# Kernel tuning notes

Hardware: AMD Instinct MI355X
Metric: run time of the kernel (lower is better)

The kernel has to match this reference:

```python
import jax, jax.numpy as jnp
import numpy as np
import math

B, S, HID = 128, 200, 1024
NH = 4
DK = HID // NH
LSESS = 200  # session_len
MAXSEQ = 200
EPS = 1e-12


def setup_inputs() -> dict:
    key = jax.random.key(0)
    ks = jax.random.split(key, 12)
    inp = {}
    inp['query'] = jax.random.normal(ks[0], (B, S, HID), jnp.float32)
    inp['key'] = jax.random.normal(ks[1], (B, S, HID), jnp.float32)
    inp['value'] = jax.random.normal(ks[2], (B, S, HID), jnp.float32)
    std = 0.05
    inp['attn_w0'] = std * jax.random.normal(ks[3], (DK, DK), jnp.float32)
    inp['attn_w1'] = std * jax.random.normal(ks[4], (DK, DK), jnp.float32)
    inp['attn_w2'] = std * jax.random.normal(ks[5], (DK, DK), jnp.float32)
    inp['attn_w3'] = std * jax.random.normal(ks[6], (LSESS, DK), jnp.float32)
    inp['attn_bias'] = jnp.zeros((DK,), jnp.float32)
    inp['complex_weight'] = 0.02 * jax.random.normal(ks[7], (1, NH, MAXSEQ // 2 + 1, DK, 2), jnp.float32)
    bound = 1.0 / math.sqrt(HID)
    inp['linear_w'] = jax.random.uniform(ks[8], (HID, HID), jnp.float32, -bound, bound)
    inp['linear_b'] = jax.random.uniform(ks[9], (HID,), jnp.float32, -bound, bound)
    inp['ln_w'] = jnp.ones((HID,), jnp.float32)
    inp['ln_b'] = jnp.zeros((HID,), jnp.float32)
    return inp


def _gelu(x):
    return x * 0.5 * (1.0 + jax.lax.erf(x / jnp.sqrt(jnp.asarray(2.0, x.dtype))))


def reference(query, key, value, attn_w0, attn_w1, attn_w2, attn_w3, attn_bias,
              complex_weight, linear_w, linear_b, ln_w, ln_b):
    nb = query.shape[0]
    # (B, S, H, DK) -> (B, H, S, DK)
    def split_heads(x):
        return x.reshape(nb, -1, NH, DK).transpose(0, 2, 1, 3)
    q, k, v = split_heads(query), split_heads(key), split_heads(value)

    q = q @ attn_w0
    k = k @ attn_w1
    v = v @ attn_w2

    qf = jnp.fft.rfft(q, axis=2, norm='ortho')   # (B,H,S//2+1,DK) complex
    kf = jnp.fft.rfft(k, axis=2, norm='ortho')
    weight = complex_weight[..., 0] + 1j * complex_weight[..., 1]  # (1,4,MAXSEQ//2+1,DK)
    res = qf * jnp.conj(kf) * weight
    corr = jnp.fft.irfft(res, n=MAXSEQ, axis=2, norm='ortho')       # (B,H,MAXSEQ,DK)

    alpha = jnp.matmul(jax.nn.relu(corr + attn_bias), attn_w3.T)    # (B,H,MAXSEQ,LSESS)
    alpha = jax.nn.softmax(alpha, axis=-2)                          # softmax over seq dim
    x = jnp.einsum('bhsl,bhsd->bhld', alpha, v)                     # (B,H,LSESS,DK)

    x = x.transpose(0, 2, 1, 3).reshape(nb, -1, NH * DK)            # (B,LSESS,HID)
    x = x @ linear_w.T + linear_b
    # dropout is identity at inference
    x = _gelu(x)
    # LayerNorm (TF-style, eps inside sqrt)
    u = x.mean(-1, keepdims=True)
    s = ((x - u) ** 2).mean(-1, keepdims=True)
    x = (x - u) / jnp.sqrt(s + EPS)
    return ln_w * x + ln_b
```

## Files before the change

### kernel.cpp

```cpp
#include <hip/hip_runtime.h>
#include <hip/hip_bf16.h>
#include <math.h>

#define BATCH 128
#define SEQ   200
#define HID   1024
#define NH    4
#define DK    256
#define NF    101
#define NF2   202
#define LS    200
#define PD    256

typedef __attribute__((ext_vector_type(8))) short bf16x8;
typedef __attribute__((ext_vector_type(4))) float f32x4;

__device__ __forceinline__ unsigned short f2bf(float f) {
    union { float f; unsigned u; } v; v.f = f;
    unsigned r = v.u + 0x7fff + ((v.u >> 16) & 1);
    return (unsigned short)(r >> 16);
}
__device__ __forceinline__ float bf2f(unsigned short h) {
    union { unsigned u; float f; } v; v.u = ((unsigned)h) << 16;
    return v.f;
}

__device__ __forceinline__ void gld_lds16(const void* g, void* l) {
    __builtin_amdgcn_global_load_lds(
        (const __attribute__((address_space(1))) unsigned*)g,
        (__attribute__((address_space(3))) unsigned*)l, 16, 0, 0);
}

__global__ void init_tables_bf16(unsigned short* __restrict__ F, unsigned short* __restrict__ G) {
    int idx = blockIdx.x * 256 + threadIdx.x;
    const double inv = 0.07071067811865475244;
    const double PI2 = 6.283185307179586476925;
    {
        int fidx = idx >> 8, s = idx & 255;
        double v = 0.0;
        if (s < SEQ && fidx < NF2) {
            int f = (fidx < NF) ? fidx : fidx - NF;
            double ang = PI2 * (double)((f * s) % SEQ) / (double)SEQ;
            v = (fidx < NF) ? cos(ang) * inv : -sin(ang) * inv;
        }
        F[idx] = f2bf((float)v);
    }
    {
        int s = idx >> 8, j = idx & 255;
        double v = 0.0;
        if (s < SEQ && j < NF2) {
            if (j < NF) {
                double al = (j == 0 || j == NF - 1) ? 1.0 : 2.0;
                v = al * cos(PI2 * (double)((j * s) % SEQ) / (double)SEQ) * inv;
            } else {
                int f = j - NF;
                if (f != 0 && f != NF - 1)
                    v = -2.0 * sin(PI2 * (double)((f * s) % SEQ) / (double)SEQ) * inv;
            }
        }
        G[idx] = f2bf((float)v);
    }
}

__global__ void wtrans256(const float* __restrict__ src, unsigned short* __restrict__ dst) {
    int dout = blockIdx.x, din = threadIdx.x;
    dst[dout * 256 + din] = f2bf(src[din * 256 + dout]);
}

__global__ void w3pad(const float* __restrict__ src, unsigned short* __restrict__ dst) {
    int row = blockIdx.x, col = threadIdx.x;
    dst[row * 256 + col] = (row < LS) ? f2bf(src[row * 256 + col]) : (unsigned short)0;
}

__global__ void fconv(const float* __restrict__ src, unsigned short* __restrict__ dst, int n) {
    int i = blockIdx.x * 256 + threadIdx.x;
    if (i < n) dst[i] = f2bf(src[i]);
}

template <bool B_F32, int EPI>
__global__ __launch_bounds__(256)
void mgemm128(const void* __restrict__ Av, const void* __restrict__ Bv, void* __restrict__ Cv,
              int K, int lda, int ldb, int ldc,
              long aOuter, long aInner, long bOuter, long bInner,
              long cOuter, long cInner, int nInner, int nbValid,
              const float* __restrict__ biasN) {
    int bz = blockIdx.z;
    int bo = bz / nInner, bi = bz - bo * nInner;
    const unsigned short* A = (const unsigned short*)Av + bo * aOuter + bi * aInner;
    const unsigned short* Bh = nullptr;
    const float* Bf = nullptr;
    if (B_F32) Bf = (const float*)Bv + bo * bOuter + bi * bInner;
    else       Bh = (const unsigned short*)Bv + bo * bOuter + bi * bInner;

    __shared__ unsigned short As[128 * 64];
    __shared__ unsigned short Bs[128 * 64];

    int t = threadIdx.x;
    int m0 = blockIdx.y * 128, n0 = blockIdx.x * 128;
    int lane = t & 63, wave = t >> 6;
    int wr = wave >> 1, wc = wave & 1;
    int la = lane & 15, hi = lane >> 4;

    f32x4 acc[4][4] = {};

    int rsub = t >> 3;
    int c8 = (t & 7) * 8;

    for (int k0 = 0; k0 < K; k0 += 64) {
#pragma unroll
        for (int p = 0; p < 4; ++p) {
            int row = p * 32 + rsub;
            gld_lds16(A + (long)(m0 + row) * lda + k0 + c8, &As[row * 64 + c8]);
        }
        if (!B_F32) {
#pragma unroll
            for (int p = 0; p < 4; ++p) {
                int row = p * 32 + rsub;
                gld_lds16(Bh + (long)(n0 + row) * ldb + k0 + c8, &Bs[row * 64 + c8]);
            }
        } else {
#pragma unroll
            for (int p = 0; p < 4; ++p) {
                int row = p * 32 + rsub;
                int gn = n0 + row;
                unsigned short tmp[8];
                if (gn < nbValid) {
                    const float4* src = reinterpret_cast<const float4*>(Bf + (long)gn * ldb + k0 + c8);
                    float4 x0 = src[0], x1 = src[1];
                    tmp[0] = f2bf(x0.x); tmp[1] = f2bf(x0.y); tmp[2] = f2bf(x0.z); tmp[3] = f2bf(x0.w);
                    tmp[4] = f2bf(x1.x); tmp[5] = f2bf(x1.y); tmp[6] = f2bf(x1.z); tmp[7] = f2bf(x1.w);
                } else {
#pragma unroll
                    for (int j = 0; j < 8; ++j) tmp[j] = 0;
                }
                *(bf16x8*)&Bs[row * 64 + c8] = *(bf16x8*)tmp;
            }
        }
        __syncthreads();
#pragma unroll
        for (int half = 0; half < 2; ++half) {
            int ko = half * 32 + hi * 8;
            bf16x8 a[4], b[4];
#pragma unroll
            for (int mi = 0; mi < 4; ++mi)
                a[mi] = *(const bf16x8*)&As[(wr * 64 + mi * 16 + la) * 64 + ko];
#pragma unroll
            for (int ni = 0; ni < 4; ++ni)
                b[ni] = *(const bf16x8*)&Bs[(wc * 64 + ni * 16 + la) * 64 + ko];
#pragma unroll
            for (int mi = 0; mi < 4; ++mi)
#pragma unroll
                for (int ni = 0; ni < 4; ++ni)
                    acc[mi][ni] = __builtin_amdgcn_mfma_f32_16x16x32_bf16(a[mi], b[ni], acc[mi][ni], 0, 0, 0);
        }
        __syncthreads();
    }

    unsigned short* Ch = nullptr; float* Cf = nullptr;
    if (EPI == 1 || EPI == 3) Cf = (float*)Cv + bo * cOuter + bi * cInner;
    else                      Ch = (unsigned short*)Cv + bo * cOuter + bi * cInner;

#pragma unroll
    for (int mi = 0; mi < 4; ++mi) {
#pragma unroll
        for (int ni = 0; ni < 4; ++ni) {
            int gn = n0 + wc * 64 + ni * 16 + la;
            int gmB = m0 + wr * 64 + mi * 16 + hi * 4;
            float bN = 0.f;
            if (EPI == 2 || EPI == 3) bN = biasN[gn];
#pragma unroll
            for (int rr = 0; rr < 4; ++rr) {
                float v = acc[mi][ni][rr];
                long idx = (long)(gmB + rr) * ldc + gn;
                if (EPI == 0) Ch[idx] = f2bf(v);
                else if (EPI == 1) Cf[idx] = v;
                else if (EPI == 2) Ch[idx] = f2bf(fmaxf(v + bN, 0.f));
                else Cf[idx] = v + bN;
            }
        }
    }
}

__global__ void crossspec(unsigned short* __restrict__ QF, const unsigned short* __restrict__ KF,
                          const float* __restrict__ cw) {
    long idx = (long)blockIdx.x * 256 + threadIdx.x;
    if (idx >= (long)BATCH * NH * DK * NF) return;
    int f = (int)(idx % NF);
    long tq = idx / NF;
    int d = (int)(tq % DK);
    int bh = (int)(tq / DK);
    int h = bh & (NH - 1);
    long base = (long)bh * DK * PD + (long)d * PD;
    float qr = bf2f(QF[base + f]), qi = bf2f(QF[base + NF + f]);
    float kr = bf2f(KF[base + f]), ki = bf2f(KF[base + NF + f]);
    float cr = qr * kr + qi * ki;
    float ci = qi * kr - qr * ki;
    long wb = (((long)h * NF + f) * DK + d) * 2;
    float wr = cw[wb], wi = cw[wb + 1];
    QF[base + f]      = f2bf(cr * wr - ci * wi);
    QF[base + NF + f] = f2bf(cr * wi + ci * wr);
    if (f < PD - NF2) QF[base + NF2 + f] = 0;
}

__global__ __launch_bounds__(256) void softmax_rows(const float* __restrict__ in,
                                                    unsigned short* __restrict__ out) {
    long row = (long)blockIdx.x * 4 + (threadIdx.x >> 6);
    int lane = threadIdx.x & 63;
    const float* p = in + row * PD;
    float v[4];
    float m = -1e30f;
#pragma unroll
    for (int i = 0; i < 4; ++i) {
        int s = lane + 64 * i;
        v[i] = (s < SEQ) ? p[s] : -1e30f;
        m = fmaxf(m, v[i]);
    }
#pragma unroll
    for (int o = 32; o; o >>= 1) m = fmaxf(m, __shfl_xor(m, o));
    float e[4], sum = 0.f;
#pragma unroll
    for (int i = 0; i < 4; ++i) {
        int s = lane + 64 * i;
        e[i] = (s < SEQ) ? expf(v[i] - m) : 0.f;
        sum += e[i];
    }
#pragma unroll
    for (int o = 32; o; o >>= 1) sum += __shfl_xor(sum, o);
    float inv = 1.f / sum;
    unsigned short* q = out + row * PD;
#pragma unroll
    for (int i = 0; i < 4; ++i) {
        int s = lane + 64 * i;
        q[s] = (s < SEQ) ? f2bf(e[i] * inv) : (unsigned short)0;
    }
}

__global__ __launch_bounds__(256) void transposeX(const unsigned short* __restrict__ xT,
                                                  unsigned short* __restrict__ X) {
    __shared__ unsigned short T[64][72];
    int bh = blockIdx.z, d0 = blockIdx.y * 64, l0 = blockIdx.x * 64;
    int b = bh >> 2, h = bh & 3;
    int t = threadIdx.x;
    int r = t >> 2, seg = (t & 3) * 16;
    const unsigned short* src = xT + (long)bh * PD * PD + (long)(d0 + r) * PD + l0 + seg;
    *(bf16x8*)&T[r][seg]     = *(const bf16x8*)(src);
    *(bf16x8*)&T[r][seg + 8] = *(const bf16x8*)(src + 8);
    __syncthreads();
    int l = l0 + r;
    if (l < LS) {
        unsigned short* dst = X + ((long)b * LS + l) * HID + h * DK + d0 + seg;
#pragma unroll
        for (int j = 0; j < 16; ++j) dst[j] = T[seg + j][r];
    }
}

__global__ __launch_bounds__(256) void gelu_ln_kernel(const float* __restrict__ y2,
                               const float* __restrict__ lnw, const float* __restrict__ lnb,
                               float* __restrict__ out) {
    long row = blockIdx.x;
    const float4* xr = reinterpret_cast<const float4*>(y2 + row * HID);
    int tid = threadIdx.x;
    float4 v4 = xr[tid];
    float g[4];
    g[0] = 0.5f * v4.x * (1.f + erff(v4.x * 0.70710678118654752f));
    g[1] = 0.5f * v4.y * (1.f + erff(v4.y * 0.70710678118654752f));
    g[2] = 0.5f * v4.z * (1.f + erff(v4.z * 0.70710678118654752f));
    g[3] = 0.5f * v4.w * (1.f + erff(v4.w * 0.70710678118654752f));

    __shared__ float red[4];
    float s = g[0] + g[1] + g[2] + g[3];
#pragma unroll
    for (int o = 32; o > 0; o >>= 1) s += __shfl_down(s, o);
    if ((tid & 63) == 0) red[tid >> 6] = s;
    __syncthreads();
    float mean = (red[0] + red[1] + red[2] + red[3]) * (1.f / (float)HID);

    float v2 = 0.f;
#pragma unroll
    for (int p = 0; p < 4; ++p) { float d = g[p] - mean; v2 += d * d; }
    __syncthreads();
#pragma unroll
    for (int o = 32; o > 0; o >>= 1) v2 += __shfl_down(v2, o);
    if ((tid & 63) == 0) red[tid >> 6] = v2;
    __syncthreads();
    float var = (red[0] + red[1] + red[2] + red[3]) * (1.f / (float)HID);
    float rstd = rsqrtf(var + 1e-12f);

    float4 o4;
    int i0 = tid * 4;
    o4.x = (g[0] - mean) * rstd * lnw[i0 + 0] + lnb[i0 + 0];
    o4.y = (g[1] - mean) * rstd * lnw[i0 + 1] + lnb[i0 + 1];
    o4.z = (g[2] - mean) * rstd * lnw[i0 + 2] + lnb[i0 + 2];
    o4.w = (g[3] - mean) * rstd * lnw[i0 + 3] + lnb[i0 + 3];
    reinterpret_cast<float4*>(out + row * HID)[tid] = o4;
}

extern "C" void kernel_launch(void* const* d_in, const int* in_sizes, int n_in,
                              void* d_out, int out_size, void* d_ws, size_t ws_size,
                              hipStream_t stream) {
    const float* query = (const float*)d_in[0];
    const float* key   = (const float*)d_in[1];
    const float* value = (const float*)d_in[2];
    const float* w0 = (const float*)d_in[3];
    const float* w1 = (const float*)d_in[4];
    const float* w2 = (const float*)d_in[5];
    const float* w3 = (const float*)d_in[6];
    const float* attn_bias = (const float*)d_in[7];
    const float* cw = (const float*)d_in[8];
    const float* lw = (const float*)d_in[9];
    const float* lb = (const float*)d_in[10];
    const float* lnw = (const float*)d_in[11];
    const float* lnb = (const float*)d_in[12];
    float* out = (float*)d_out;

    char* base = (char*)d_ws;
    const long BH = (long)BATCH * NH;
    const long SZR = (long)BH * PD * PD;
    const size_t M64 = 67108864;

    unsigned short* F_stack = (unsigned short*)(base + 0);
    unsigned short* G_stack = (unsigned short*)(base + 131072);
    unsigned short* w0T = (unsigned short*)(base + 262144);
    unsigned short* w1T = (unsigned short*)(base + 393216);
    unsigned short* w2T = (unsigned short*)(base + 524288);
    unsigned short* w3b = (unsigned short*)(base + 655360);
    unsigned short* lwb = (unsigned short*)(base + 786432);
    char* rA = base + 4194304;
    char* rB = rA + M64;
    char* rC = rB + M64;
    char* rD = rC + M64;
    char* rE = rD + M64;

    unsigned short* qpT = (unsigned short*)rA;
    unsigned short* kpT = (unsigned short*)rB;
    unsigned short* vpT = (unsigned short*)rC;
    unsigned short* QF  = (unsigned short*)rD;
    unsigned short* KF  = (unsigned short*)rE;
    unsigned short* corr = (unsigned short*)rA;
    float*          alphaT = (float*)rD;
    unsigned short* probs = (unsigned short*)rB;
    unsigned short* xT = (unsigned short*)rE;
    unsigned short* X  = (unsigned short*)rA;
    float*          y2 = (float*)rD;

    init_tables_bf16<<<256, 256, 0, stream>>>(F_stack, G_stack);
    wtrans256<<<256, 256, 0, stream>>>(w0, w0T);
    wtrans256<<<256, 256, 0, stream>>>(w1, w1T);
    wtrans256<<<256, 256, 0, stream>>>(w2, w2T);
    w3pad<<<256, 256, 0, stream>>>(w3, w3b);
    fconv<<<(HID * HID + 255) / 256, 256, 0, stream>>>(lw, lwb, HID * HID);

    dim3 gproj(2, 2, BH);
    mgemm128<true, 0><<<gproj, 256, 0, stream>>>(w0T, query, qpT, DK, DK, HID, PD,
        0L, 0L, (long)SEQ * HID, (long)DK, (long)NH * PD * PD, (long)PD * PD, NH, SEQ, nullptr);
    mgemm128<true, 0><<<gproj, 256, 0, stream>>>(w1T, key, kpT, DK, DK, HID, PD,
        0L, 0L, (long)SEQ * HID, (long)DK, (long)NH * PD * PD, (long)PD * PD, NH, SEQ, nullptr);
    mgemm128<true, 0><<<gproj, 256, 0, stream>>>(w2T, value, vpT, DK, DK, HID, PD,
        0L, 0L, (long)SEQ * HID, (long)DK, (long)NH * PD * PD, (long)PD * PD, NH, SEQ, nullptr);

    dim3 gfwd(2, 2, 2 * BH);
    mgemm128<false, 0><<<gfwd, 256, 0, stream>>>(qpT, F_stack, QF, PD, PD, PD, PD,
        SZR, (long)PD * PD, 0L, 0L, SZR, (long)PD * PD, (int)BH, PD, nullptr);

    long ncs = (long)BH * DK * NF;
    crossspec<<<(unsigned)((ncs + 255) / 256), 256, 0, stream>>>(QF, KF, cw);

    dim3 gstd(2, 2, BH);
    mgemm128<false, 2><<<gstd, 256, 0, stream>>>(G_stack, QF, corr, PD, PD, PD, PD,
        0L, 0L, (long)PD * PD, 0L, (long)PD * PD, 0L, 1, PD, attn_bias);

    mgemm128<false, 1><<<gstd, 256, 0, stream>>>(w3b, corr, alphaT, PD, PD, PD, PD,
        0L, 0L, (long)PD * PD, 0L, (long)PD * PD, 0L, 1, PD, nullptr);

    softmax_rows<<<(unsigned)(BH * PD / 4), 256, 0, stream>>>(alphaT, probs);

    mgemm128<false, 0><<<gstd, 256, 0, stream>>>(vpT, probs, xT, PD, PD, PD, PD,
        (long)PD * PD, 0L, (long)PD * PD, 0L, (long)PD * PD, 0L, 1, PD, nullptr);

    transposeX<<<dim3(4, 4, BH), 256, 0, stream>>>(xT, X);

    dim3 glin(HID / 128, (BATCH * LS) / 128, 1);
    mgemm128<false, 3><<<glin, 256, 0, stream>>>(X, lwb, y2, HID, HID, HID, HID,
        0L, 0L, 0L, 0L, 0L, 0L, 1, HID, lb);

    gelu_ln_kernel<<<(unsigned)(BATCH * LS), 256, 0, stream>>>(y2, lnw, lnb, out);
}
```

Before: 720.5 us.

## Double-buffer bf16 GEMMs, fuse transpose into attention GEMM, store intermediates as bf16

Adds a double-buffered LDS GEMM variant that prefetches the next K tile while computing the current one. It switches alpha and the linear output from fp32 to bf16 storage, which halves their memory traffic. The value GEMM is reordered to write directly in (B,LS,HID) layout, so the separate transpose kernel is no longer needed. The big linear GEMM gets an XCD-aware block swizzle. The costs are lower precision on the softmax input and on the GELU/LN input, plus twice the shared memory per block.

```diff
diff --git a/kernel.cpp b/kernel.cpp
--- a/kernel.cpp
+++ b/kernel.cpp
@@ -77,20 +77,16 @@
     if (i < n) dst[i] = f2bf(src[i]);
 }
 
-template <bool B_F32, int EPI>
 __global__ __launch_bounds__(256)
-void mgemm128(const void* __restrict__ Av, const void* __restrict__ Bv, void* __restrict__ Cv,
+void mgemm128(const unsigned short* __restrict__ A, const float* __restrict__ Bf0,
+              unsigned short* __restrict__ C0,
               int K, int lda, int ldb, int ldc,
               long aOuter, long aInner, long bOuter, long bInner,
-              long cOuter, long cInner, int nInner, int nbValid,
-              const float* __restrict__ biasN) {
+              long cOuter, long cInner, int nInner, int nbValid) {
     int bz = blockIdx.z;
     int bo = bz / nInner, bi = bz - bo * nInner;
-    const unsigned short* A = (const unsigned short*)Av + bo * aOuter + bi * aInner;
-    const unsigned short* Bh = nullptr;
-    const float* Bf = nullptr;
-    if (B_F32) Bf = (const float*)Bv + bo * bOuter + bi * bInner;
-    else       Bh = (const unsigned short*)Bv + bo * bOuter + bi * bInner;
+    const unsigned short* Ab = A + bo * aOuter + bi * aInner;
+    const float* Bf = Bf0 + bo * bOuter + bi * bInner;
 
     __shared__ unsigned short As[128 * 64];
     __shared__ unsigned short Bs[128 * 64];
@@ -102,7 +98,6 @@
     int la = lane & 15, hi = lane >> 4;
 
     f32x4 acc[4][4] = {};
-
     int rsub = t >> 3;
     int c8 = (t & 7) * 8;
 
@@ -110,31 +105,23 @@
 #pragma unroll
         for (int p = 0; p < 4; ++p) {
             int row = p * 32 + rsub;
-            gld_lds16(A + (long)(m0 + row) * lda + k0 + c8, &As[row * 64 + c8]);
-        }
-        if (!B_F32) {
-#pragma unroll
-            for (int p = 0; p < 4; ++p) {
-                int row = p * 32 + rsub;
-                gld_lds16(Bh + (long)(n0 + row) * ldb + k0 + c8, &Bs[row * 64 + c8]);
+            gld_lds16(Ab + (long)(m0 + row) * lda + k0 + c8, &As[row * 64 + c8]);
+        }
+#pragma unroll
+        for (int p = 0; p < 4; ++p) {
+            int row = p * 32 + rsub;
+            int gn = n0 + row;
+            unsigned short tmp[8];
+            if (gn < nbValid) {
+                const float4* src = reinterpret_cast<const float4*>(Bf + (long)gn * ldb + k0 + c8);
+                float4 x0 = src[0], x1 = src[1];
+                tmp[0] = f2bf(x0.x); tmp[1] = f2bf(x0.y); tmp[2] = f2bf(x0.z); tmp[3] = f2bf(x0.w);
+                tmp[4] = f2bf(x1.x); tmp[5] = f2bf(x1.y); tmp[6] = f2bf(x1.z); tmp[7] = f2bf(x1.w);
+            } else {
+#pragma unroll
+                for (int j = 0; j < 8; ++j) tmp[j] = 0;
             }
-        } else {
-#pragma unroll
-            for (int p = 0; p < 4; ++p) {
-                int row = p * 32 + rsub;
-                int gn = n0 + row;
-                unsigned short tmp[8];
-                if (gn < nbValid) {
-                    const float4* src = reinterpret_cast<const float4*>(Bf + (long)gn * ldb + k0 + c8);
-                    float4 x0 = src[0], x1 = src[1];
-                    tmp[0] = f2bf(x0.x); tmp[1] = f2bf(x0.y); tmp[2] = f2bf(x0.z); tmp[3] = f2bf(x0.w);
-                    tmp[4] = f2bf(x1.x); tmp[5] = f2bf(x1.y); tmp[6] = f2bf(x1.z); tmp[7] = f2bf(x1.w);
-                } else {
-#pragma unroll
-                    for (int j = 0; j < 8; ++j) tmp[j] = 0;
-                }
-                *(bf16x8*)&Bs[row * 64 + c8] = *(bf16x8*)tmp;
-            }
+            *(bf16x8*)&Bs[row * 64 + c8] = *(bf16x8*)tmp;
         }
         __syncthreads();
 #pragma unroll
@@ -156,10 +143,96 @@
         __syncthreads();
     }
 
-    unsigned short* Ch = nullptr; float* Cf = nullptr;
-    if (EPI == 1 || EPI == 3) Cf = (float*)Cv + bo * cOuter + bi * cInner;
-    else                      Ch = (unsigned short*)Cv + bo * cOuter + bi * cInner;
-
+    unsigned short* Ch = C0 + bo * cOuter + bi * cInner;
+#pragma unroll
+    for (int mi = 0; mi < 4; ++mi) {
+#pragma unroll
+        for (int ni = 0; ni < 4; ++ni) {
+            int gn = n0 + wc * 64 + ni * 16 + la;
+            int gmB = m0 + wr * 64 + mi * 16 + hi * 4;
+#pragma unroll
+            for (int rr = 0; rr < 4; ++rr)
+                Ch[(long)(gmB + rr) * ldc + gn] = f2bf(acc[mi][ni][rr]);
+        }
+    }
+}
+
+template <int EPI, bool XCDSWZ>
+__global__ __launch_bounds__(256)
+void mgemm128p(const unsigned short* __restrict__ A, const unsigned short* __restrict__ B,
+               unsigned short* __restrict__ C0, int K, int lda, int ldb, int ldc,
+               long aOuter, long aInner, long bOuter, long bInner,
+               long cOuter, long cInner, int nInner, int mValid,
+               const float* __restrict__ biasN) {
+    int bx = blockIdx.x, by = blockIdx.y;
+    if (XCDSWZ) {
+        int nwg = gridDim.x * gridDim.y;
+        int flat = by * gridDim.x + bx;
+        int cpx = nwg >> 3;
+        int swz = (flat & 7) * cpx + (flat >> 3);
+        bx = swz % gridDim.x; by = swz / gridDim.x;
+    }
+    int bz = blockIdx.z;
+    int bo = bz / nInner, bi = bz - bo * nInner;
+    const unsigned short* Ab = A + bo * aOuter + bi * aInner;
+    const unsigned short* Bb = B + bo * bOuter + bi * bInner;
+
+    __shared__ unsigned short As[2][128 * 64];
+    __shared__ unsigned short Bs[2][128 * 64];
+
+    int t = threadIdx.x;
+    int m0 = by * 128, n0 = bx * 128;
+    int lane = t & 63, wave = t >> 6;
+    int wr = wave >> 1, wc = wave & 1;
+    int la = lane & 15, hi = lane >> 4;
+
+    f32x4 acc[4][4] = {};
+    int rsub = t >> 3;
+    int c8 = (t & 7) * 8;
+
+    int ktiles = K >> 6;
+
+#pragma unroll
+    for (int p = 0; p < 4; ++p) {
+        int row = p * 32 + rsub;
+        gld_lds16(Ab + (long)(m0 + row) * lda + c8, &As[0][row * 64 + c8]);
+        gld_lds16(Bb + (long)(n0 + row) * ldb + c8, &Bs[0][row * 64 + c8]);
+    }
+    __syncthreads();
+
+    int cur = 0;
+    for (int kt = 0; kt < ktiles; ++kt) {
+        if (kt + 1 < ktiles) {
+            int k0 = (kt + 1) << 6;
+            int nxt = cur ^ 1;
+#pragma unroll
+            for (int p = 0; p < 4; ++p) {
+                int row = p * 32 + rsub;
+                gld_lds16(Ab + (long)(m0 + row) * lda + k0 + c8, &As[nxt][row * 64 + c8]);
+                gld_lds16(Bb + (long)(n0 + row) * ldb + k0 + c8, &Bs[nxt][row * 64 + c8]);
+            }
+        }
+#pragma unroll
+        for (int half = 0; half < 2; ++half) {
+            int ko = half * 32 + hi * 8;
+            bf16x8 a[4], b[4];
+#pragma unroll
+            for (int mi = 0; mi < 4; ++mi)
+                a[mi] = *(const bf16x8*)&As[cur][(wr * 64 + mi * 16 + la) * 64 + ko];
+#pragma unroll
+            for (int ni = 0; ni < 4; ++ni)
+                b[ni] = *(const bf16x8*)&Bs[cur][(wc * 64 + ni * 16 + la) * 64 + ko];
+#pragma unroll
+            for (int mi = 0; mi < 4; ++mi)
+#pragma unroll
+                for (int ni = 0; ni < 4; ++ni)
+                    acc[mi][ni] = __builtin_amdgcn_mfma_f32_16x16x32_bf16(a[mi], b[ni], acc[mi][ni], 0, 0, 0);
+        }
+        __syncthreads();
+        cur ^= 1;
+    }
+
+    unsigned short* Ch = C0 + bo * cOuter + bi * cInner;
 #pragma unroll
     for (int mi = 0; mi < 4; ++mi) {
 #pragma unroll
@@ -167,15 +240,15 @@
             int gn = n0 + wc * 64 + ni * 16 + la;
             int gmB = m0 + wr * 64 + mi * 16 + hi * 4;
             float bN = 0.f;
-            if (EPI == 2 || EPI == 3) bN = biasN[gn];
+            if (EPI == 2 || EPI == 4) bN = biasN[gn];
 #pragma unroll
             for (int rr = 0; rr < 4; ++rr) {
+                int gm = gmB + rr;
+                if (gm >= mValid) continue;
                 float v = acc[mi][ni][rr];
-                long idx = (long)(gmB + rr) * ldc + gn;
-                if (EPI == 0) Ch[idx] = f2bf(v);
-                else if (EPI == 1) Cf[idx] = v;
-                else if (EPI == 2) Ch[idx] = f2bf(fmaxf(v + bN, 0.f));
-                else Cf[idx] = v + bN;
+                if (EPI == 0) Ch[(long)gm * ldc + gn] = f2bf(v);
+                else if (EPI == 2) Ch[(long)gm * ldc + gn] = f2bf(fmaxf(v + bN, 0.f));
+                else Ch[(long)gm * ldc + gn] = f2bf(v + bN);
             }
         }
     }
@@ -202,17 +275,17 @@
     if (f < PD - NF2) QF[base + NF2 + f] = 0;
 }
 
-__global__ __launch_bounds__(256) void softmax_rows(const float* __restrict__ in,
+__global__ __launch_bounds__(256) void softmax_rows(const unsigned short* __restrict__ in,
                                                     unsigned short* __restrict__ out) {
     long row = (long)blockIdx.x * 4 + (threadIdx.x >> 6);
     int lane = threadIdx.x & 63;
-    const float* p = in + row * PD;
+    const unsigned short* p = in + row * PD;
     float v[4];
     float m = -1e30f;
 #pragma unroll
     for (int i = 0; i < 4; ++i) {
         int s = lane + 64 * i;
-        v[i] = (s < SEQ) ? p[s] : -1e30f;
+        v[i] = (s < SEQ) ? bf2f(p[s]) : -1e30f;
         m = fmaxf(m, v[i]);
     }
 #pragma unroll
@@ -235,37 +308,22 @@
     }
 }
 
-__global__ __launch_bounds__(256) void transposeX(const unsigned short* __restrict__ xT,
-                                                  unsigned short* __restrict__ X) {
-    __shared__ unsigned short T[64][72];
-    int bh = blockIdx.z, d0 = blockIdx.y * 64, l0 = blockIdx.x * 64;
-    int b = bh >> 2, h = bh & 3;
-    int t = threadIdx.x;
-    int r = t >> 2, seg = (t & 3) * 16;
-    const unsigned short* src = xT + (long)bh * PD * PD + (long)(d0 + r) * PD + l0 + seg;
-    *(bf16x8*)&T[r][seg]     = *(const bf16x8*)(src);
-    *(bf16x8*)&T[r][seg + 8] = *(const bf16x8*)(src + 8);
-    __syncthreads();
-    int l = l0 + r;
-    if (l < LS) {
-        unsigned short* dst = X + ((long)b * LS + l) * HID + h * DK + d0 + seg;
-#pragma unroll
-        for (int j = 0; j < 16; ++j) dst[j] = T[seg + j][r];
-    }
-}
-
-__global__ __launch_bounds__(256) void gelu_ln_kernel(const float* __restrict__ y2,
+__global__ __launch_bounds__(256) void gelu_ln_kernel(const unsigned short* __restrict__ y2,
                                const float* __restrict__ lnw, const float* __restrict__ lnb,
                                float* __restrict__ out) {
     long row = blockIdx.x;
-    const float4* xr = reinterpret_cast<const float4*>(y2 + row * HID);
     int tid = threadIdx.x;
-    float4 v4 = xr[tid];
+    const short4* xr = reinterpret_cast<const short4*>(y2 + row * HID);
+    short4 h4 = xr[tid];
     float g[4];
-    g[0] = 0.5f * v4.x * (1.f + erff(v4.x * 0.70710678118654752f));
-    g[1] = 0.5f * v4.y * (1.f + erff(v4.y * 0.70710678118654752f));
-    g[2] = 0.5f * v4.z * (1.f + erff(v4.z * 0.70710678118654752f));
-    g[3] = 0.5f * v4.w * (1.f + erff(v4.w * 0.70710678118654752f));
+    {
+        float x0 = bf2f((unsigned short)h4.x), x1 = bf2f((unsigned short)h4.y);
+        float x2 = bf2f((unsigned short)h4.z), x3 = bf2f((unsigned short)h4.w);
+        g[0] = 0.5f * x0 * (1.f + erff(x0 * 0.70710678118654752f));
+        g[1] = 0.5f * x1 * (1.f + erff(x1 * 0.70710678118654752f));
+        g[2] = 0.5f * x2 * (1.f + erff(x2 * 0.70710678118654752f));
+        g[3] = 0.5f * x3 * (1.f + erff(x3 * 0.70710678118654752f));
+    }
 
     __shared__ float red[4];
     float s = g[0] + g[1] + g[2] + g[3];
@@ -337,11 +395,10 @@
     unsigned short* QF  = (unsigned short*)rD;
     unsigned short* KF  = (unsigned short*)rE;
     unsigned short* corr = (unsigned short*)rA;
-    float*          alphaT = (float*)rD;
+    unsigned short* alphaT = (unsigned short*)rD;
     unsigned short* probs = (unsigned short*)rB;
-    unsigned short* xT = (unsigned short*)rE;
-    unsigned short* X  = (unsigned short*)rA;
-    float*          y2 = (float*)rD;
+    unsigned short* X  = (unsigned short*)rE;
+    unsigned short* y2 = (unsigned short*)rD;
 
     init_tables_bf16<<<256, 256, 0, stream>>>(F_stack, G_stack);
     wtrans256<<<256, 256, 0, stream>>>(w0, w0T);
@@ -351,37 +408,37 @@
     fconv<<<(HID * HID + 255) / 256, 256, 0, stream>>>(lw, lwb, HID * HID);
 
     dim3 gproj(2, 2, BH);
-    mgemm128<true, 0><<<gproj, 256, 0, stream>>>(w0T, query, qpT, DK, DK, HID, PD,
-        0L, 0L, (long)SEQ * HID, (long)DK, (long)NH * PD * PD, (long)PD * PD, NH, SEQ, nullptr);
-    mgemm128<true, 0><<<gproj, 256, 0, stream>>>(w1T, key, kpT, DK, DK, HID, PD,
-        0L, 0L, (long)SEQ * HID, (long)DK, (long)NH * PD * PD, (long)PD * PD, NH, SEQ, nullptr);
-    mgemm128<true, 0><<<gproj, 256, 0, stream>>>(w2T, value, vpT, DK, DK, HID, PD,
-        0L, 0L, (long)SEQ * HID, (long)DK, (long)NH * PD * PD, (long)PD * PD, NH, SEQ, nullptr);
+    mgemm128<<<gproj, 256, 0, stream>>>(w0T, query, qpT, DK, DK, HID, PD,
+        0L, 0L, (long)SEQ * HID, (long)DK, (long)NH * PD * PD, (long)PD * PD, NH, SEQ);
+    mgemm128<<<gproj, 256, 0, stream>>>(w1T, key, kpT, DK, DK, HID, PD,
+        0L, 0L, (long)SEQ * HID, (long)DK, (long)NH * PD * PD, (long)PD * PD, NH, SEQ);
+    mgemm128<<<gproj, 256, 0, stream>>>(w2T, value, vpT, DK, DK, HID, PD,
+        0L, 0L, (long)SEQ * HID, (long)DK, (long)NH * PD * PD, (long)PD * PD, NH, SEQ);
 
     dim3 gfwd(2, 2, 2 * BH);
-    mgemm128<false, 0><<<gfwd, 256, 0, stream>>>(qpT, F_stack, QF, PD, PD, PD, PD,
+    mgemm128p<0, false><<<gfwd, 256, 0, stream>>>(qpT, F_stack, QF, PD, PD, PD, PD,
         SZR, (long)PD * PD, 0L, 0L, SZR, (long)PD * PD, (int)BH, PD, nullptr);
 
     long ncs = (long)BH * DK * NF;
     crossspec<<<(unsigned)((ncs + 255) / 256), 256, 0, stream>>>(QF, KF, cw);
 
     dim3 gstd(2, 2, BH);
-    mgemm128<false, 2><<<gstd, 256, 0, stream>>>(G_stack, QF, corr, PD, PD, PD, PD,
+    mgemm128p<2, false><<<gstd, 256, 0, stream>>>(G_stack, QF, corr, PD, PD, PD, PD,
         0L, 0L, (long)PD * PD, 0L, (long)PD * PD, 0L, 1, PD, attn_bias);
 
-    mgemm128<false, 1><<<gstd, 256, 0, stream>>>(w3b, corr, alphaT, PD, PD, PD, PD,
+    mgemm128p<0, false><<<gstd, 256, 0, stream>>>(w3b, corr, alphaT, PD, PD, PD, PD,
         0L, 0L, (long)PD * PD, 0L, (long)PD * PD, 0L, 1, PD, nullptr);
 
     softmax_rows<<<(unsigned)(BH * PD / 4), 256, 0, stream>>>(alphaT, probs);
 
-    mgemm128<false, 0><<<gstd, 256, 0, stream>>>(vpT, probs, xT, PD, PD, PD, PD,
-        (long)PD * PD, 0L, (long)PD * PD, 0L, (long)PD * PD, 0L, 1, PD, nullptr);
-
-    transposeX<<<dim3(4, 4, BH), 256, 0, stream>>>(xT, X);
+    mgemm128p<0, false><<<gstd, 256, 0, stream>>>(probs, vpT, X, PD, PD, PD, HID,
+        (long)NH * PD * PD, (long)PD * PD,
+        (long)NH * PD * PD, (long)PD * PD,
+        (long)LS * HID, (long)DK, NH, LS, nullptr);
 
     dim3 glin(HID / 128, (BATCH * LS) / 128, 1);
-    mgemm128<false, 3><<<glin, 256, 0, stream>>>(X, lwb, y2, HID, HID, HID, HID,
-        0L, 0L, 0L, 0L, 0L, 0L, 1, HID, lb);
+    mgemm128p<4, true><<<glin, 256, 0, stream>>>(X, lwb, y2, HID, HID, HID, HID,
+        0L, 0L, 0L, 0L, 0L, 0L, 1, BATCH * LS, lb);
 
     gelu_ln_kernel<<<(unsigned)(BATCH * LS), 256, 0, stream>>>(y2, lnw, lnb, out);
 }
```

Result: slower. 738.2 us (+2.5%).
